# Performance work log

Hardware: AMD Instinct MI355X
Metric: run time of the kernel (lower is better)

Reference implementation:

```python
import jax, jax.numpy as jnp
import numpy as np
from jax import lax

EPOCHS = 3
KS = [2, 3, 4, 5]
GRID_D = 5           # sqrt(25): covariance viewed as 5x5 grid of flat indices
M_OUT = 18           # AttentionManifold output SPD size

def _sub_idx(d, k):
    # flat indices of k*k x k*k principal submatrices (stride-1 windows), per SubManifold
    starts = np.arange(0, d - k + 1)
    ir, ic = np.meshgrid(starts, starts, indexing='ij')
    base = (ir * d + ic).reshape(-1)                       # [num_windows]
    a, b = np.meshgrid(np.arange(k), np.arange(k), indexing='ij')
    rel = (a * d + b).reshape(-1)                          # [k*k]
    return base[:, None] + rel[None, :]                    # [num_windows, k*k]

SUB_IDX = [_sub_idx(GRID_D, k) for k in KS]
IN_DIMS = [k * k for k in KS]                              # [4, 9, 16, 25]
IU = np.triu_indices(M_OUT)                                # 171 tangent features
TRI_COEF = np.where(IU[0] == IU[1], 1.0, np.sqrt(2.0)).astype(np.float32)

def _sym_fn(x, fn):
    w, u = jnp.linalg.eigh(x)
    return jnp.einsum('...ik,...k,...jk->...ij', u, fn(w), u)

def spd_log(x, floor=1e-9):
    # matrix log of SPD matrix (== torch.svd-based log for PD input)
    return _sym_fn(x, lambda w: jnp.log(jnp.clip(w, floor)))

def spd_exp(x):
    return _sym_fn(x, jnp.exp)

def spd_rect(x, eps=1e-4):
    # SPDRectified (ReEig): clamp eigenvalues from below
    return _sym_fn(x, lambda w: jnp.clip(w, eps))

def bimap(X, W):
    # SPDTransform: W^T X W, W: [d_in, d_out]
    return jnp.einsum('ia,...ij,jb->...ab', W, X, W)

def diag_jitter(x):
    # deterministic analogue of the random diagonal jitter in SubmanifoldAttention.tensor_log
    n = x.shape[-1]
    return x + jnp.diag((1e-4 / n) * (1.0 + jnp.arange(n, dtype=x.dtype)))

def signal2spd(x):
    # x: [B, C, T] -> trace-normalized covariance [B, C, C]
    x = x - x.mean(-1, keepdims=True)
    cov = jnp.einsum('bct,bdt->bcd', x, x) / (x.shape[-1] - 1)
    tra = jnp.trace(cov, axis1=-2, axis2=-1)[:, None, None]
    cov = cov / tra
    return cov + 1e-5 * jnp.eye(cov.shape[-1], dtype=cov.dtype)

def spd_attention(Q, K, V, jitter):
    # log-maps computed once per element; pairwise log-Euclidean distance via Frobenius identity
    if jitter:
        Q, K, V = diag_jitter(Q), diag_jitter(K), diag_jitter(V)
    logQ, logK = spd_log(Q), spd_log(K)
    qn = jnp.sum(logQ * logQ, (-2, -1))                    # [B, m]
    kn = jnp.sum(logK * logK, (-2, -1))
    cross = jnp.einsum('bixy,bjxy->bij', logK, logQ)
    # E[b,i,j] = ||logQ_j - logK_i||_F^2  (sum of singular values of D D^T)
    E = jnp.maximum(kn[:, :, None] + qn[:, None, :] - 2.0 * cross, 0.0)
    score = 1.0 / (1.0 + jnp.log1p(E))
    P = jnp.swapaxes(jax.nn.softmax(score, axis=-2), -1, -2)  # softmax over i, then permute
    B, m, sz, _ = V.shape
    logV = spd_log(V).reshape(B, m, sz * sz)
    out_log = (P @ logV).reshape(B, m, sz, sz)             # log-Euclidean weighted mean
    out_log = 0.5 * (out_log + jnp.swapaxes(out_log, -1, -2))
    return spd_exp(out_log)

def _bn(y, g, b, m, v):
    inv = g / jnp.sqrt(v + 1e-5)
    return (y - m[None, :, None, None]) * inv[None, :, None, None] + b[None, :, None, None]

def _forward(x, c1w, c1b, bn1g, bn1b, bn1m, bn1v, c2w, c2b, bn2g, bn2b, bn2m, bn2v,
             sq0, sq1, sq2, sq3, sk0, sk1, sk2, sk3, sv0, sv1, sv2, sv3,
             mq, mk, mv, lw, lb):
    dn = ('NCHW', 'OIHW', 'NCHW')
    y = lax.conv_general_dilated(x, c1w, (1, 1), 'VALID', dimension_numbers=dn) + c1b[None, :, None, None]
    y = _bn(y, bn1g, bn1b, bn1m, bn1v)
    y = lax.conv_general_dilated(y, c2w, (1, 1), [(0, 0), (6, 6)], dimension_numbers=dn) + c2b[None, :, None, None]
    y = _bn(y, bn2g, bn2b, bn2m, bn2v)
    sig = y[:, :, 0, :]                                    # squeeze -> [B, 25, T+1]
    T = sig.shape[-1]
    base = T // EPOCHS
    lens = [base + (1 if i < T - base * EPOCHS else 0) for i in range(EPOCHS)]
    covs, off = [], 0
    for Lp in lens:
        covs.append(signal2spd(sig[..., off:off + Lp])); off += Lp
    covs = jnp.stack(covs, axis=1)                         # [B, 3, 25, 25]
    sqs = [sq0, sq1, sq2, sq3]; sks = [sk0, sk1, sk2, sk3]; svs = [sv0, sv1, sv2, sv3]
    branch = []
    for t in range(EPOCHS):
        xb = covs[:, t]                                    # [B, 25, 25]
        Qs, Ks, Vs = [], [], []
        for gi, idx in enumerate(SUB_IDX):
            sub = xb[:, idx[:, :, None], idx[:, None, :]]  # [B, nw, k*k, k*k]
            Qs.append(bimap(sub, sqs[gi]))
            Ks.append(bimap(sub, sks[gi]))
            Vs.append(bimap(sub, svs[gi]))
        att = spd_attention(jnp.concatenate(Qs, 1), jnp.concatenate(Ks, 1),
                            jnp.concatenate(Vs, 1), jitter=True)   # [B, 30, 25, 25]
        branch.append(spd_rect(att[:, -1]))                # keep_only_last
    xm = jnp.stack(branch, axis=1)                         # [B, 3, 25, 25]
    att2 = spd_attention(bimap(xm, mq), bimap(xm, mk), bimap(xm, mv), jitter=False)
    Lg = spd_log(spd_rect(att2))                           # [B, 3, 18, 18]
    feat = (Lg[..., IU[0], IU[1]] * jnp.asarray(TRI_COEF)).reshape(xm.shape[0], -1)
    return feat @ lw.T + lb                                # [B, 4]

def setup_inputs():
    B, T = 256, 1000
    key = jax.random.key(0)
    ks = jax.random.split(key, 40)
    def ortho(k, din, dout):
        a = jax.random.normal(k, (max(din, dout), min(din, dout)), dtype=jnp.float32)
        q, _ = jnp.linalg.qr(a)
        return q if din >= dout else q.T
    inp = {
        'x': jax.random.normal(ks[0], (B, 1, 22, T), dtype=jnp.float32),
        'c1w': 0.1 * jax.random.normal(ks[1], (22, 1, 22, 1), dtype=jnp.float32),
        'c1b': 0.01 * jax.random.normal(ks[2], (22,), dtype=jnp.float32),
        'bn1g': 1.0 + 0.1 * jax.random.normal(ks[3], (22,), dtype=jnp.float32),
        'bn1b': 0.01 * jax.random.normal(ks[4], (22,), dtype=jnp.float32),
        'bn1m': 0.1 * jax.random.normal(ks[5], (22,), dtype=jnp.float32),
        'bn1v': 0.5 + jax.random.uniform(ks[6], (22,), dtype=jnp.float32),
        'c2w': 0.05 * jax.random.normal(ks[7], (25, 22, 1, 12), dtype=jnp.float32),
        'c2b': 0.01 * jax.random.normal(ks[8], (25,), dtype=jnp.float32),
        'bn2g': 1.0 + 0.1 * jax.random.normal(ks[9], (25,), dtype=jnp.float32),
        'bn2b': 0.01 * jax.random.normal(ks[10], (25,), dtype=jnp.float32),
        'bn2m': 0.1 * jax.random.normal(ks[11], (25,), dtype=jnp.float32),
        'bn2v': 0.5 + jax.random.uniform(ks[12], (25,), dtype=jnp.float32),
    }
    for i, din in enumerate(IN_DIMS):
        inp[f'sq{i}'] = ortho(ks[13 + i], din, 4)
        inp[f'sk{i}'] = ortho(ks[17 + i], din, 4)
        inp[f'sv{i}'] = ortho(ks[21 + i], din, 25)
    inp['mq'] = ortho(ks[25], 25, 18)
    inp['mk'] = ortho(ks[26], 25, 18)
    inp['mv'] = ortho(ks[27], 25, 18)
    inp['lw'] = 0.05 * jax.random.normal(ks[28], (4, EPOCHS * len(IU[0])), dtype=jnp.float32)
    inp['lb'] = 0.01 * jax.random.normal(ks[29], (4,), dtype=jnp.float32)
    return inp

def reference(x, c1w, c1b, bn1g, bn1b, bn1m, bn1v, c2w, c2b, bn2g, bn2b, bn2m, bn2v,
              sq0, sq1, sq2, sq3, sk0, sk1, sk2, sk3, sv0, sv1, sv2, sv3,
              mq, mk, mv, lw, lb):
    return _forward(x, c1w, c1b, bn1g, bn1b, bn1m, bn1v, c2w, c2b, bn2g, bn2b, bn2m, bn2v,
                    sq0, sq1, sq2, sq3, sk0, sk1, sk2, sk3, sv0, sv1, sv2, sv3,
                    mq, mk, mv, lw, lb)
```

## Files before the change

kernel.cpp:

```cpp
#include <hip/hip_runtime.h>
#include <hip/hip_bf16.h>
#include <math.h>


__global__ __launch_bounds__(256) void conv1_kernel(
    const float* __restrict__ x, const float* __restrict__ c1w, const float* __restrict__ c1b,
    const float* __restrict__ g, const float* __restrict__ be, const float* __restrict__ mu,
    const float* __restrict__ va, float* __restrict__ ybn1)
{
  __shared__ float w[484];
  __shared__ float scl[22], sft[22];
  int t = threadIdx.x;
  for (int e = t; e < 484; e += 256) w[e] = c1w[e];
  if (t < 22) { float inv = g[t] / sqrtf(va[t] + 1e-5f); scl[t] = inv; sft[t] = be[t] - mu[t]*inv; }
  __syncthreads();
  int gid = blockIdx.x*256 + t;
  int b = gid / 1000, wp = gid % 1000;
  const float* xb = x + (size_t)b*22000 + wp;
  float acc[22];
  #pragma unroll
  for (int o = 0; o < 22; ++o) acc[o] = c1b[o];
  for (int h = 0; h < 22; ++h) {
    float xv = xb[h*1000];
    #pragma unroll
    for (int o = 0; o < 22; ++o) acc[o] += xv * w[o*22 + h];
  }
  float* yb = ybn1 + (size_t)b*22000 + wp;
  #pragma unroll
  for (int o = 0; o < 22; ++o) yb[o*1000] = acc[o]*scl[o] + sft[o];
}

__global__ __launch_bounds__(256) void conv2_kernel(
    const float* __restrict__ ybn1, const float* __restrict__ c2w, const float* __restrict__ c2b,
    const float* __restrict__ g, const float* __restrict__ be, const float* __restrict__ mu,
    const float* __restrict__ va, float* __restrict__ sig)
{
  __shared__ float w[6600];
  __shared__ float scl[25], sft[25];
  int t = threadIdx.x;
  for (int e = t; e < 6600; e += 256) w[e] = c2w[e];
  if (t < 25) { float inv = g[t] / sqrtf(va[t] + 1e-5f); scl[t] = inv; sft[t] = be[t] - mu[t]*inv; }
  __syncthreads();
  int gid = blockIdx.x*256 + t;
  if (gid >= 256*1001) return;
  int b = gid / 1001, wp = gid % 1001;
  const float* yb = ybn1 + (size_t)b*22000;
  float acc[25];
  #pragma unroll
  for (int p = 0; p < 25; ++p) acc[p] = c2b[p];
  for (int c = 0; c < 22; ++c) {
    for (int kw = 0; kw < 12; ++kw) {
      int wi = wp - 6 + kw;
      if (wi < 0 || wi >= 1000) continue;
      float v = yb[c*1000 + wi];
      #pragma unroll
      for (int p = 0; p < 25; ++p) acc[p] += v * w[p*264 + c*12 + kw];
    }
  }
  float* sb = sig + (size_t)b*25025 + wp;
  #pragma unroll
  for (int p = 0; p < 25; ++p) sb[p*1001] = acc[p]*scl[p] + sft[p];
}

__global__ __launch_bounds__(256) void spd_kernel(const float* __restrict__ sig, float* __restrict__ covs)
{
  __shared__ float s[25*334];
  __shared__ float mean[25];
  __shared__ float cv[625];
  __shared__ float tra;
  int bt = blockIdx.x; int b = bt/3, ep = bt%3;
  int off = ep*334;
  int Lp = (ep < 2) ? 334 : 333;
  int t = threadIdx.x;
  const float* sb = sig + (size_t)b*25025;
  for (int e = t; e < 25*Lp; e += 256) { int c = e / Lp, tt = e % Lp; s[c*334 + tt] = sb[c*1001 + off + tt]; }
  __syncthreads();
  if (t < 25) { float m = 0.f; for (int i = 0; i < Lp; ++i) m += s[t*334 + i]; mean[t] = m / (float)Lp; }
  __syncthreads();
  for (int pi = t; pi < 325; pi += 256) {
    int i = 0, rem = pi;
    while (rem >= 25 - i) { rem -= 25 - i; ++i; }
    int j = i + rem;
    float mi = mean[i], mj = mean[j], acc = 0.f;
    for (int k = 0; k < Lp; ++k) acc += (s[i*334 + k] - mi) * (s[j*334 + k] - mj);
    float v = acc / (float)(Lp - 1);
    cv[i*25 + j] = v; cv[j*25 + i] = v;
  }
  __syncthreads();
  if (t == 0) { float tr = 0.f; for (int i = 0; i < 25; ++i) tr += cv[i*26]; tra = tr; }
  __syncthreads();
  float inv = 1.f / tra;
  for (int e = t; e < 625; e += 256) {
    int i = e / 25, j = e % 25;
    covs[(size_t)bt*625 + e] = cv[e]*inv + ((i == j) ? 1e-5f : 0.f);
  }
}

__global__ __launch_bounds__(64) void build_windows_kernel(
    const float* __restrict__ covs,
    const float* __restrict__ sk0, const float* __restrict__ sk1, const float* __restrict__ sk2, const float* __restrict__ sk3,
    const float* __restrict__ sv0, const float* __restrict__ sv1, const float* __restrict__ sv2, const float* __restrict__ sv3,
    const float* __restrict__ sq3,
    float* __restrict__ Vbuf, float* __restrict__ Kbuf, float* __restrict__ Qbuf)
{
  __shared__ float sSub[625], sSv[625], sTmp[625], sSk[100], sTk[100];
  int bw = blockIdx.x;
  int bt = bw / 30, win = bw % 30;
  int t = threadIdx.x;
  int k, r0, c0;
  const float* sv; const float* sk;
  if (win < 16)      { k = 2; r0 = win/4;        c0 = win%4;        sv = sv0; sk = sk0; }
  else if (win < 25) { k = 3; int u = win-16; r0 = u/3; c0 = u%3;   sv = sv1; sk = sk1; }
  else if (win < 29) { k = 4; int u = win-25; r0 = u/2; c0 = u%2;   sv = sv2; sk = sk2; }
  else               { k = 5; r0 = 0;            c0 = 0;            sv = sv3; sk = sk3; }
  int kk = k*k;
  const float* cov = covs + (size_t)bt*625;
  for (int e = t; e < kk*kk; e += 64) {
    int p = e / kk, q = e % kk;
    int ip = (r0 + p/k)*5 + (c0 + p%k);
    int iq = (r0 + q/k)*5 + (c0 + q%k);
    sSub[p*kk + q] = cov[ip*25 + iq];
  }
  for (int e = t; e < kk*25; e += 64) sSv[e] = sv[e];
  for (int e = t; e < kk*4; e += 64)  sSk[e] = sk[e];
  __syncthreads();
  for (int e = t; e < kk*25; e += 64) {
    int i = e / 25, b = e % 25;
    float acc = 0.f;
    for (int j = 0; j < kk; ++j) acc += sSub[i*kk + j] * sSv[j*25 + b];
    sTmp[e] = acc;
  }
  for (int e = t; e < kk*4; e += 64) {
    int i = e / 4, b = e % 4;
    float acc = 0.f;
    for (int j = 0; j < kk; ++j) acc += sSub[i*kk + j] * sSk[j*4 + b];
    sTk[e] = acc;
  }
  __syncthreads();
  float* Vout = Vbuf + (size_t)bw*625;
  for (int e = t; e < 625; e += 64) {
    int a = e / 25, b = e % 25;
    float acc = 0.f;
    for (int i = 0; i < kk; ++i) acc += sSv[i*25 + a] * sTmp[i*25 + b];
    if (a == b) acc += 4e-6f * (float)(1 + a);
    Vout[e] = acc;
  }
  float* Kout = Kbuf + (size_t)bw*16;
  for (int e = t; e < 16; e += 64) {
    int a = e / 4, b = e % 4;
    float acc = 0.f;
    for (int i = 0; i < kk; ++i) acc += sSk[i*4 + a] * sTk[i*4 + b];
    if (a == b) acc += 2.5e-5f * (float)(1 + a);
    Kout[e] = acc;
  }
  if (win == 29) {
    __syncthreads();
    for (int e = t; e < 100; e += 64) {
      int i = e / 4, b = e % 4;
      float acc = 0.f;
      for (int j = 0; j < 25; ++j) acc += sSub[i*25 + j] * sq3[j*4 + b];
      sTk[e] = acc;
    }
    __syncthreads();
    float* Qout = Qbuf + (size_t)bt*16;
    for (int e = t; e < 16; e += 64) {
      int a = e / 4, b = e % 4;
      float acc = 0.f;
      for (int i = 0; i < 25; ++i) acc += sq3[i*4 + a] * sTk[i*4 + b];
      if (a == b) acc += 2.5e-5f * (float)(1 + a);
      Qout[e] = acc;
    }
  }
}

template<int NDATA, int MODE, int SHIFT>
__global__ __launch_bounds__(64) void eighreg_kernel(float* __restrict__ mats, float* __restrict__ norms_out)
{
  constexpr int NPAD = (NDATA + 1) & ~1;
  constexpr int NR   = NPAD - 1;
  constexpr int LDW  = NPAD + 1;
  constexpr int NT   = NDATA*(NDATA+1)/2;

  __shared__ float lds[2*NDATA*LDW];
  __shared__ float wvs[64];

  int t = threadIdx.x;
  int half = t >> 5;
  int col  = t & 31;
  int base32 = t & 32;
  float* M = mats + (size_t)blockIdx.x*2*NDATA*NDATA;

  for (int e = t; e < 2*NDATA*NDATA; e += 64) lds[e] = M[e];
  __syncthreads();

  const float* st = lds + half*NDATA*NDATA;
  float own[NDATA];
  float n_own = 0.f;
  #pragma unroll
  for (int r = 0; r < NDATA; ++r) {
    float v = 0.f;
    if (col < NDATA) {
      v = 0.5f*(st[r*NDATA + col] + st[col*NDATA + r]);
      if (r == col) v += (float)SHIFT;
    }
    own[r] = v;
    n_own += v*v;
  }
  __syncthreads();

  for (int sw = 0; sw < 12; ++sw) {
    float relacc = 0.f;
    #pragma unroll 1
    for (int r = 0; r < NR; ++r) {
      int p2 = 2*r - col;
      p2 += (p2 < 0) ? NR : 0;
      p2 -= (p2 >= NR) ? NR : 0;
      p2 = (col == r) ? (NPAD-1) : p2;
      p2 = (col == NPAD-1) ? r : p2;
      int idx = (base32 + p2) * 4;
      float y[NDATA];
      float d = 0.f;
      #pragma unroll
      for (int r2 = 0; r2 < NDATA; ++r2) {
        float yv = __int_as_float(__builtin_amdgcn_ds_bpermute(idx, __float_as_int(own[r2])));
        y[r2] = yv;
        d = fmaf(own[r2], yv, d);
      }
      float n_other = __int_as_float(__builtin_amdgcn_ds_bpermute(idx, __float_as_int(n_own)));
      float ad = fabsf(d);
      float dd = (ad > 1e-36f) ? d : 1e-36f;
      float tau = (n_other - n_own) * 0.5f * __builtin_amdgcn_rcpf(dd);
      float mag = __builtin_amdgcn_rcpf(fabsf(tau) + sqrtf(tau*tau + 1.f));
      float tt = copysignf(mag, tau);
      float c = __builtin_amdgcn_rsqf(tt*tt + 1.f);
      float s = tt * c;
      #pragma unroll
      for (int r2 = 0; r2 < NDATA; ++r2) own[r2] = c*own[r2] - s*y[r2];
      relacc = fmaxf(relacc, d*d * __builtin_amdgcn_rcpf(fmaxf(n_own*n_other, 1e-30f)));
      n_own = c*c*n_own + s*s*n_other - 2.f*c*s*d;
    }
    float nn = 0.f;
    #pragma unroll
    for (int r2 = 0; r2 < NDATA; ++r2) nn = fmaf(own[r2], own[r2], nn);
    n_own = nn;
    if (sw >= 1 && !__any(relacc >= 9e-10f)) break;
  }

  float lam = sqrtf(n_own) - (float)SHIFT;
  float f;
  if (MODE == 0)      f = logf(fmaxf(lam, 1e-9f));
  else if (MODE == 1) f = fmaxf(expf(lam), 1e-4f);
  else                f = fmaxf(lam, -9.210340371976182f);
  wvs[t] = (n_own < 1e-30f) ? 0.f : f * __builtin_amdgcn_rcpf(n_own);

  float* gn = lds + half*NDATA*LDW;
  if (col < NPAD) {
    #pragma unroll
    for (int r2 = 0; r2 < NDATA; ++r2) gn[r2*LDW + col] = own[r2];
  }
  __syncthreads();

  const float* wm = wvs + base32;
  float* Mo = M + half*NDATA*NDATA;
  float nacc = 0.f;
  for (int e = col; e < NT; e += 32) {
    int i = 0, rem = e;
    while (rem >= NDATA - i) { rem -= NDATA - i; ++i; }
    int j = i + rem;
    float acc = 0.f;
    #pragma unroll
    for (int k = 0; k < NDATA; ++k) acc += wm[k]*gn[i*LDW + k]*gn[j*LDW + k];
    Mo[i*NDATA + j] = acc;
    Mo[j*NDATA + i] = acc;
    nacc += (i == j) ? acc*acc : 2.f*acc*acc;
  }
  if (norms_out != nullptr) {
    #pragma unroll
    for (int o = 16; o > 0; o >>= 1) nacc += __shfl_xor(nacc, o);
    if (col == 0) norms_out[blockIdx.x*2 + half] = nacc;
  }
}

template<int P, int Q>
__device__ __forceinline__ void rot4(float a[4][4], float u[4][4])
{
  float apq = a[P][Q];
  if (fabsf(apq) < 1e-36f) return;
  float app = a[P][P], aqq = a[Q][Q];
  float tau = (aqq - app) / (2.f*apq);
  float tt = 1.f / (fabsf(tau) + sqrtf(tau*tau + 1.f));
  if (tau < 0.f) tt = -tt;
  float c = 1.f / sqrtf(tt*tt + 1.f), s = tt*c;
  #pragma unroll
  for (int k = 0; k < 4; ++k) { float akp = a[k][P], akq = a[k][Q]; a[k][P] = c*akp - s*akq; a[k][Q] = s*akp + c*akq; }
  #pragma unroll
  for (int k = 0; k < 4; ++k) { float apk = a[P][k], aqk = a[Q][k]; a[P][k] = c*apk - s*aqk; a[Q][k] = s*apk + c*aqk; }
  #pragma unroll
  for (int k = 0; k < 4; ++k) { float ukp = u[k][P], ukq = u[k][Q]; u[k][P] = c*ukp - s*ukq; u[k][Q] = s*ukp + c*ukq; }
}

__global__ __launch_bounds__(256) void eigh4_kernel(float* __restrict__ kmats, float* __restrict__ qmats,
                                                    float* __restrict__ norms)
{
  int idx = blockIdx.x*256 + threadIdx.x;
  if (idx >= 23808) return;
  float* M = (idx < 23040) ? (kmats + (size_t)idx*16) : (qmats + (size_t)(idx - 23040)*16);
  float a[4][4], u[4][4];
  #pragma unroll
  for (int i = 0; i < 4; ++i)
    #pragma unroll
    for (int j = 0; j < 4; ++j) { a[i][j] = 0.5f*(M[i*4+j] + M[j*4+i]); u[i][j] = (i == j) ? 1.f : 0.f; }
  #pragma unroll 1
  for (int sw = 0; sw < 8; ++sw) {
    rot4<0,1>(a,u); rot4<0,2>(a,u); rot4<0,3>(a,u);
    rot4<1,2>(a,u); rot4<1,3>(a,u); rot4<2,3>(a,u);
  }
  float f[4];
  #pragma unroll
  for (int i = 0; i < 4; ++i) f[i] = logf(fmaxf(a[i][i], 1e-9f));
  float nrm = 0.f;
  #pragma unroll
  for (int i = 0; i < 4; ++i)
    #pragma unroll
    for (int j = 0; j < 4; ++j) {
      float acc = 0.f;
      #pragma unroll
      for (int k = 0; k < 4; ++k) acc += u[i][k]*f[k]*u[j][k];
      M[i*4+j] = acc; nrm += acc*acc;
    }
  norms[idx] = nrm;
}

__global__ __launch_bounds__(64) void att1_kernel(
    const float* __restrict__ logK, const float* __restrict__ logQ,
    const float* __restrict__ kn, const float* __restrict__ qn,
    const float* __restrict__ logV, float* __restrict__ outlog1)
{
  __shared__ float lq[16];
  __shared__ float sscore[30];
  __shared__ float sp[30];
  int bt = blockIdx.x, t = threadIdx.x;
  if (t < 16) lq[t] = logQ[(size_t)bt*16 + t];
  __syncthreads();
  if (t < 30) {
    const float* lk = logK + ((size_t)bt*30 + t)*16;
    float cr = 0.f;
    #pragma unroll
    for (int e = 0; e < 16; ++e) cr += lk[e]*lq[e];
    float E = fmaxf(kn[bt*30 + t] + qn[bt] - 2.f*cr, 0.f);
    sscore[t] = 1.f/(1.f + log1pf(E));
  }
  __syncthreads();
  float mx = -1e30f;
  for (int i = 0; i < 30; ++i) mx = fmaxf(mx, sscore[i]);
  float sm = 0.f;
  for (int i = 0; i < 30; ++i) sm += expf(sscore[i] - mx);
  if (t < 30) sp[t] = expf(sscore[t] - mx)/sm;
  __syncthreads();
  const float* lv = logV + (size_t)bt*30*625;
  float* outp = outlog1 + (size_t)bt*625;
  for (int e = t; e < 625; e += 64) {
    float acc = 0.f;
    for (int i = 0; i < 30; ++i) acc += sp[i]*lv[(size_t)i*625 + e];
    outp[e] = acc;
  }
}

__global__ __launch_bounds__(64) void qkv2_kernel(
    const float* __restrict__ xm, const float* __restrict__ mq, const float* __restrict__ mk,
    const float* __restrict__ mv, float* __restrict__ q2, float* __restrict__ k2, float* __restrict__ v2)
{
  __shared__ float sx[625], sw[450], stmp[450];
  int bt = blockIdx.x, t = threadIdx.x;
  for (int e = t; e < 625; e += 64) sx[e] = xm[(size_t)bt*625 + e];
  for (int wi = 0; wi < 3; ++wi) {
    const float* W = (wi == 0) ? mq : (wi == 1) ? mk : mv;
    float* O = ((wi == 0) ? q2 : (wi == 1) ? k2 : v2) + (size_t)bt*324;
    for (int e = t; e < 450; e += 64) sw[e] = W[e];
    __syncthreads();
    for (int e = t; e < 450; e += 64) {
      int i = e / 18, b = e % 18;
      float acc = 0.f;
      for (int j = 0; j < 25; ++j) acc += sx[i*25 + j]*sw[j*18 + b];
      stmp[e] = acc;
    }
    __syncthreads();
    for (int e = t; e < 324; e += 64) {
      int a = e / 18, b = e % 18;
      float acc = 0.f;
      for (int i = 0; i < 25; ++i) acc += sw[i*18 + a]*stmp[i*18 + b];
      O[e] = acc;
    }
    __syncthreads();
  }
}

__global__ __launch_bounds__(64) void att2_kernel(
    const float* __restrict__ logQ2, const float* __restrict__ logK2, const float* __restrict__ logV2,
    const float* __restrict__ norms, float* __restrict__ outlog2)
{
  __shared__ float S[3][3];
  __shared__ float PT[3][3];
  int b = blockIdx.x, t = threadIdx.x;
  if (t < 9) {
    int i = t / 3, j = t % 3;
    const float* lk = logK2 + ((size_t)b*3 + i)*324;
    const float* lq = logQ2 + ((size_t)b*3 + j)*324;
    float cr = 0.f;
    for (int e = 0; e < 324; ++e) cr += lk[e]*lq[e];
    float E = fmaxf(norms[768 + b*3 + i] + norms[b*3 + j] - 2.f*cr, 0.f);
    S[i][j] = 1.f/(1.f + log1pf(E));
  }
  __syncthreads();
  if (t < 3) {
    float m = fmaxf(S[0][t], fmaxf(S[1][t], S[2][t]));
    float e0 = expf(S[0][t]-m), e1 = expf(S[1][t]-m), e2 = expf(S[2][t]-m);
    float ssum = e0 + e1 + e2;
    PT[t][0] = e0/ssum; PT[t][1] = e1/ssum; PT[t][2] = e2/ssum;
  }
  __syncthreads();
  for (int e = t; e < 324; e += 64) {
    float l0 = logV2[((size_t)b*3 + 0)*324 + e];
    float l1 = logV2[((size_t)b*3 + 1)*324 + e];
    float l2 = logV2[((size_t)b*3 + 2)*324 + e];
    #pragma unroll
    for (int j = 0; j < 3; ++j)
      outlog2[((size_t)b*3 + j)*324 + e] = PT[j][0]*l0 + PT[j][1]*l1 + PT[j][2]*l2;
  }
}

__global__ __launch_bounds__(64) void feat_kernel(
    const float* __restrict__ Lg, const float* __restrict__ lw, const float* __restrict__ lb,
    float* __restrict__ outp)
{
  __shared__ int tri_i[171], tri_j[171];
  int b = blockIdx.x, t = threadIdx.x;
  if (t == 0) { int f = 0; for (int i = 0; i < 18; ++i) for (int j = i; j < 18; ++j) { tri_i[f] = i; tri_j[f] = j; ++f; } }
  __syncthreads();
  float a0 = 0.f, a1 = 0.f, a2 = 0.f, a3 = 0.f;
  const float SQ2 = 1.41421356237309515f;
  for (int f = t; f < 513; f += 64) {
    int tt = f / 171, r = f % 171;
    int i = tri_i[r], j = tri_j[r];
    float coef = (i == j) ? 1.f : SQ2;
    float v = Lg[((size_t)b*3 + tt)*324 + i*18 + j] * coef;
    a0 += v*lw[0*513 + f]; a1 += v*lw[1*513 + f]; a2 += v*lw[2*513 + f]; a3 += v*lw[3*513 + f];
  }
  #pragma unroll
  for (int off = 32; off > 0; off >>= 1) {
    a0 += __shfl_down(a0, off); a1 += __shfl_down(a1, off);
    a2 += __shfl_down(a2, off); a3 += __shfl_down(a3, off);
  }
  if (t == 0) {
    outp[b*4 + 0] = a0 + lb[0]; outp[b*4 + 1] = a1 + lb[1];
    outp[b*4 + 2] = a2 + lb[2]; outp[b*4 + 3] = a3 + lb[3];
  }
}

extern "C" void kernel_launch(void* const* d_in, const int* in_sizes, int n_in,
                              void* d_out, int out_size, void* d_ws, size_t ws_size,
                              hipStream_t stream)
{
  const float* x    = (const float*)d_in[0];
  const float* c1w  = (const float*)d_in[1];
  const float* c1b  = (const float*)d_in[2];
  const float* bn1g = (const float*)d_in[3];
  const float* bn1b = (const float*)d_in[4];
  const float* bn1m = (const float*)d_in[5];
  const float* bn1v = (const float*)d_in[6];
  const float* c2w  = (const float*)d_in[7];
  const float* c2b  = (const float*)d_in[8];
  const float* bn2g = (const float*)d_in[9];
  const float* bn2b = (const float*)d_in[10];
  const float* bn2m = (const float*)d_in[11];
  const float* bn2v = (const float*)d_in[12];
  const float* sk0  = (const float*)d_in[14];
  const float* sv0  = (const float*)d_in[15];
  const float* sk1  = (const float*)d_in[17];
  const float* sv1  = (const float*)d_in[18];
  const float* sk2  = (const float*)d_in[20];
  const float* sv2  = (const float*)d_in[21];
  const float* sq3  = (const float*)d_in[22];
  const float* sk3  = (const float*)d_in[23];
  const float* sv3  = (const float*)d_in[24];
  const float* mq   = (const float*)d_in[25];
  const float* mk   = (const float*)d_in[26];
  const float* mv   = (const float*)d_in[27];
  const float* lw   = (const float*)d_in[28];
  const float* lb   = (const float*)d_in[29];
  float* outp = (float*)d_out;

  float* ws = (float*)d_ws;
  float* covs = ws;
  float* ybn1 = ws + 480000;
  float* sig  = ws + 6112000;
  float* Vbuf = ws + 480000;
  float* Kbuf = ws + 14880000;
  float* Qbuf = ws + 15248640;
  float* knb  = ws + 15260928;
  float* ol1  = ws + 15284736;
  float* qkv2 = ws + 15764736;
  float* nrm2 = ws + 16511232;
  float* ol2  = ws + 16513536;

  conv1_kernel<<<1000, 256, 0, stream>>>(x, c1w, c1b, bn1g, bn1b, bn1m, bn1v, ybn1);
  conv2_kernel<<<1001, 256, 0, stream>>>(ybn1, c2w, c2b, bn2g, bn2b, bn2m, bn2v, sig);
  spd_kernel<<<768, 256, 0, stream>>>(sig, covs);
  build_windows_kernel<<<23040, 64, 0, stream>>>(covs, sk0, sk1, sk2, sk3, sv0, sv1, sv2, sv3, sq3,
                                                 Vbuf, Kbuf, Qbuf);
  eighreg_kernel<25,0,0><<<11520, 64, 0, stream>>>(Vbuf, nullptr);
  eigh4_kernel<<<93, 256, 0, stream>>>(Kbuf, Qbuf, knb);
  att1_kernel<<<768, 64, 0, stream>>>(Kbuf, Qbuf, knb, knb + 23040, Vbuf, ol1);
  eighreg_kernel<25,1,16><<<384, 64, 0, stream>>>(ol1, nullptr);
  qkv2_kernel<<<768, 64, 0, stream>>>(ol1, mq, mk, mv, qkv2, qkv2 + 248832, qkv2 + 497664);
  eighreg_kernel<18,0,0><<<1152, 64, 0, stream>>>(qkv2, nrm2);
  att2_kernel<<<256, 64, 0, stream>>>(qkv2, qkv2 + 248832, qkv2 + 497664, nrm2, ol2);
  eighreg_kernel<18,2,16><<<384, 64, 0, stream>>>(ol2, nullptr);
  feat_kernel<<<256, 64, 0, stream>>>(ol2, lw, lb, outp);
}
```

Before: 1.430 ms.

## Rewrite one-sided Jacobi eigensolver to hold two columns per lane with DPP rotation

The eigensolver now packs four matrices per 64-lane block, with each lane holding a pair of columns in registers. Instead of a bpermute exchange of a whole column every round, it rotates the pair in place and uses a DPP row shift to pass columns around a round-robin ring. This removes most LDS permute traffic and halves the number of blocks. In exchange it raises register pressure, since two 25-element columns are kept per lane, and it changes the convergence test and tolerance.

```diff
diff --git a/kernel.cpp b/kernel.cpp
--- a/kernel.cpp
+++ b/kernel.cpp
@@ -173,111 +173,171 @@
   }
 }
 
+__device__ __forceinline__ float dpp_prev(float v) {
+  return __int_as_float(__builtin_amdgcn_update_dpp(0, __float_as_int(v), 0x111, 0xF, 0xF, true));
+}
+__device__ __forceinline__ float dpp_next(float v) {
+  return __int_as_float(__builtin_amdgcn_update_dpp(0, __float_as_int(v), 0x101, 0xF, 0xF, true));
+}
+
 template<int NDATA, int MODE, int SHIFT>
-__global__ __launch_bounds__(64) void eighreg_kernel(float* __restrict__ mats, float* __restrict__ norms_out)
-{
-  constexpr int NPAD = (NDATA + 1) & ~1;
-  constexpr int NR   = NPAD - 1;
-  constexpr int LDW  = NPAD + 1;
-  constexpr int NT   = NDATA*(NDATA+1)/2;
-
-  __shared__ float lds[2*NDATA*LDW];
-  __shared__ float wvs[64];
+__global__ __launch_bounds__(64) void eighbl_kernel(float* __restrict__ mats, float* __restrict__ norms_out)
+{
+  constexpr int ND    = NDATA;
+  constexpr int NPAIR = (NDATA+1)/2;
+  constexpr int NPAD  = 2*NPAIR;
+  constexpr int NRND  = NPAD-1;
+  constexpr int NT    = ND*(ND+1)/2;
+  constexpr int STG   = 4*ND*ND;
+  constexpr int GNS   = 4*NPAD*ND;
+  constexpr int LSZ   = (STG > GNS ? STG : GNS);
+
+  __shared__ float lds[LSZ];
+  __shared__ float wv[4*NPAD];
 
   int t = threadIdx.x;
-  int half = t >> 5;
-  int col  = t & 31;
-  int base32 = t & 32;
-  float* M = mats + (size_t)blockIdx.x*2*NDATA*NDATA;
-
-  for (int e = t; e < 2*NDATA*NDATA; e += 64) lds[e] = M[e];
-  __syncthreads();
-
-  const float* st = lds + half*NDATA*NDATA;
-  float own[NDATA];
-  float n_own = 0.f;
-  #pragma unroll
-  for (int r = 0; r < NDATA; ++r) {
-    float v = 0.f;
-    if (col < NDATA) {
-      v = 0.5f*(st[r*NDATA + col] + st[col*NDATA + r]);
-      if (r == col) v += (float)SHIFT;
-    }
-    own[r] = v;
-    n_own += v*v;
-  }
-  __syncthreads();
-
+  int rl = t & 15, mat = t >> 4;
+  bool act = rl < NPAIR;
+  bool is0 = rl == 0;
+  bool isL = rl == NPAIR-1;
+  float* M = mats + (size_t)blockIdx.x*4*ND*ND;
+
+  for (int e = t; e < STG; e += 64) lds[e] = M[e];
+  __syncthreads();
+
+  const float* st = lds + mat*ND*ND;
+  int cA = rl, cB = rl + NPAIR;
+  float a[ND], b[ND];
+  float na = 0.f, nb = 0.f;
+  #pragma unroll
+  for (int i = 0; i < ND; ++i) {
+    float va = 0.f, vb = 0.f;
+    if (act) {
+      va = 0.5f*(st[i*ND + cA] + st[cA*ND + i]);
+      if (i == cA) va += (float)SHIFT;
+      if (cB < ND) {
+        vb = 0.5f*(st[i*ND + cB] + st[cB*ND + i]);
+        if (i == cB) vb += (float)SHIFT;
+      }
+    }
+    a[i] = va; b[i] = vb;
+    na += va*va; nb += vb*vb;
+  }
+
+  const float TOL2 = 4e-8f;
   for (int sw = 0; sw < 12; ++sw) {
-    float relacc = 0.f;
+    int bad = 0;
     #pragma unroll 1
-    for (int r = 0; r < NR; ++r) {
-      int p2 = 2*r - col;
-      p2 += (p2 < 0) ? NR : 0;
-      p2 -= (p2 >= NR) ? NR : 0;
-      p2 = (col == r) ? (NPAD-1) : p2;
-      p2 = (col == NPAD-1) ? r : p2;
-      int idx = (base32 + p2) * 4;
-      float y[NDATA];
-      float d = 0.f;
+    for (int r = 0; r < NRND; ++r) {
+      float d0=0.f,d1=0.f,d2=0.f,d3=0.f,d4=0.f;
       #pragma unroll
-      for (int r2 = 0; r2 < NDATA; ++r2) {
-        float yv = __int_as_float(__builtin_amdgcn_ds_bpermute(idx, __float_as_int(own[r2])));
-        y[r2] = yv;
-        d = fmaf(own[r2], yv, d);
+      for (int i = 0; i < ND; ++i) {
+        float pr = a[i]*b[i];
+        if      (i % 5 == 0) d0 += pr;
+        else if (i % 5 == 1) d1 += pr;
+        else if (i % 5 == 2) d2 += pr;
+        else if (i % 5 == 3) d3 += pr;
+        else                 d4 += pr;
       }
-      float n_other = __int_as_float(__builtin_amdgcn_ds_bpermute(idx, __float_as_int(n_own)));
+      float d = ((d0 + d1) + (d2 + d3)) + d4;
       float ad = fabsf(d);
       float dd = (ad > 1e-36f) ? d : 1e-36f;
-      float tau = (n_other - n_own) * 0.5f * __builtin_amdgcn_rcpf(dd);
+      float tau = (nb - na) * 0.5f * __builtin_amdgcn_rcpf(dd);
       float mag = __builtin_amdgcn_rcpf(fabsf(tau) + sqrtf(tau*tau + 1.f));
       float tt = copysignf(mag, tau);
       float c = __builtin_amdgcn_rsqf(tt*tt + 1.f);
       float s = tt * c;
       #pragma unroll
-      for (int r2 = 0; r2 < NDATA; ++r2) own[r2] = c*own[r2] - s*y[r2];
-      relacc = fmaxf(relacc, d*d * __builtin_amdgcn_rcpf(fmaxf(n_own*n_other, 1e-30f)));
-      n_own = c*c*n_own + s*s*n_other - 2.f*c*s*d;
-    }
-    float nn = 0.f;
-    #pragma unroll
-    for (int r2 = 0; r2 < NDATA; ++r2) nn = fmaf(own[r2], own[r2], nn);
-    n_own = nn;
-    if (sw >= 1 && !__any(relacc >= 9e-10f)) break;
-  }
-
-  float lam = sqrtf(n_own) - (float)SHIFT;
-  float f;
-  if (MODE == 0)      f = logf(fmaxf(lam, 1e-9f));
-  else if (MODE == 1) f = fmaxf(expf(lam), 1e-4f);
-  else                f = fmaxf(lam, -9.210340371976182f);
-  wvs[t] = (n_own < 1e-30f) ? 0.f : f * __builtin_amdgcn_rcpf(n_own);
-
-  float* gn = lds + half*NDATA*LDW;
-  if (col < NPAD) {
-    #pragma unroll
-    for (int r2 = 0; r2 < NDATA; ++r2) gn[r2*LDW + col] = own[r2];
-  }
-  __syncthreads();
-
-  const float* wm = wvs + base32;
-  float* Mo = M + half*NDATA*NDATA;
+      for (int i = 0; i < ND; ++i) {
+        float ta = a[i];
+        a[i] = c*ta - s*b[i];
+        b[i] = s*ta + c*b[i];
+      }
+      float csd = 2.f*c*s*d;
+      float nan_ = c*c*na + s*s*nb - csd;
+      float nbn_ = s*s*na + c*c*nb + csd;
+      bad |= (act && (d*d > TOL2*na*nb)) ? 1 : 0;
+      na = nan_; nb = nbn_;
+      #pragma unroll
+      for (int i = 0; i < ND; ++i) {
+        float tA = dpp_prev(a[i]);
+        float tB = dpp_next(b[i]);
+        float ao = a[i];
+        a[i] = is0 ? tB : tA;
+        b[i] = isL ? ao : (is0 ? b[i] : tB);
+      }
+      {
+        float tA = dpp_prev(na);
+        float tB = dpp_next(nb);
+        float ao = na;
+        na = is0 ? tB : tA;
+        nb = isL ? ao : (is0 ? nb : tB);
+      }
+    }
+    {
+      float n0=0.f,n1=0.f,n2=0.f,n3=0.f,n4=0.f;
+      float m0=0.f,m1=0.f,m2=0.f,m3=0.f,m4=0.f;
+      #pragma unroll
+      for (int i = 0; i < ND; ++i) {
+        float pa = a[i]*a[i], pb = b[i]*b[i];
+        if      (i % 5 == 0) { n0 += pa; m0 += pb; }
+        else if (i % 5 == 1) { n1 += pa; m1 += pb; }
+        else if (i % 5 == 2) { n2 += pa; m2 += pb; }
+        else if (i % 5 == 3) { n3 += pa; m3 += pb; }
+        else                 { n4 += pa; m4 += pb; }
+      }
+      na = ((n0 + n1) + (n2 + n3)) + n4;
+      nb = ((m0 + m1) + (m2 + m3)) + m4;
+    }
+    if (sw >= 1 && !__any(bad)) break;
+  }
+
+  float lamA = sqrtf(na) - (float)SHIFT;
+  float lamB = sqrtf(nb) - (float)SHIFT;
+  float fA, fB;
+  if (MODE == 0)      { fA = logf(fmaxf(lamA, 1e-9f));  fB = logf(fmaxf(lamB, 1e-9f)); }
+  else if (MODE == 1) { fA = fmaxf(expf(lamA), 1e-4f);  fB = fmaxf(expf(lamB), 1e-4f); }
+  else                { fA = fmaxf(lamA, -9.210340371976182f); fB = fmaxf(lamB, -9.210340371976182f); }
+  float wA = (na < 1e-30f) ? 0.f : fA * __builtin_amdgcn_rcpf(na);
+  float wB = (nb < 1e-30f) ? 0.f : fB * __builtin_amdgcn_rcpf(nb);
+
+  __syncthreads();
+  float* gn = lds + mat*NPAD*ND;
+  if (act) {
+    #pragma unroll
+    for (int i = 0; i < ND; ++i) {
+      gn[rl*ND + i] = a[i];
+      gn[(rl + NPAIR)*ND + i] = b[i];
+    }
+    wv[mat*NPAD + rl] = wA;
+    wv[mat*NPAD + rl + NPAIR] = wB;
+  }
+  __syncthreads();
+
+  float wreg[NPAD];
+  #pragma unroll
+  for (int k = 0; k < NPAD; ++k) wreg[k] = wv[mat*NPAD + k];
+
+  float* Mo = M + mat*ND*ND;
+  const float* g = lds + mat*NPAD*ND;
   float nacc = 0.f;
-  for (int e = col; e < NT; e += 32) {
+  for (int e = rl; e < NT; e += 16) {
     int i = 0, rem = e;
-    while (rem >= NDATA - i) { rem -= NDATA - i; ++i; }
+    while (rem >= ND - i) { rem -= ND - i; ++i; }
     int j = i + rem;
     float acc = 0.f;
     #pragma unroll
-    for (int k = 0; k < NDATA; ++k) acc += wm[k]*gn[i*LDW + k]*gn[j*LDW + k];
-    Mo[i*NDATA + j] = acc;
-    Mo[j*NDATA + i] = acc;
+    for (int k = 0; k < NPAD; ++k) acc += wreg[k] * g[k*ND + i] * g[k*ND + j];
+    Mo[i*ND + j] = acc;
+    Mo[j*ND + i] = acc;
     nacc += (i == j) ? acc*acc : 2.f*acc*acc;
   }
   if (norms_out != nullptr) {
-    #pragma unroll
-    for (int o = 16; o > 0; o >>= 1) nacc += __shfl_xor(nacc, o);
-    if (col == 0) norms_out[blockIdx.x*2 + half] = nacc;
+    nacc += __shfl_xor(nacc, 8);
+    nacc += __shfl_xor(nacc, 4);
+    nacc += __shfl_xor(nacc, 2);
+    nacc += __shfl_xor(nacc, 1);
+    if (rl == 0) norms_out[blockIdx.x*4 + mat] = nacc;
   }
 }
 
@@ -508,13 +568,13 @@
   spd_kernel<<<768, 256, 0, stream>>>(sig, covs);
   build_windows_kernel<<<23040, 64, 0, stream>>>(covs, sk0, sk1, sk2, sk3, sv0, sv1, sv2, sv3, sq3,
                                                  Vbuf, Kbuf, Qbuf);
-  eighreg_kernel<25,0,0><<<11520, 64, 0, stream>>>(Vbuf, nullptr);
+  eighbl_kernel<25,0,0><<<5760, 64, 0, stream>>>(Vbuf, nullptr);
   eigh4_kernel<<<93, 256, 0, stream>>>(Kbuf, Qbuf, knb);
   att1_kernel<<<768, 64, 0, stream>>>(Kbuf, Qbuf, knb, knb + 23040, Vbuf, ol1);
-  eighreg_kernel<25,1,16><<<384, 64, 0, stream>>>(ol1, nullptr);
+  eighbl_kernel<25,1,16><<<192, 64, 0, stream>>>(ol1, nullptr);
   qkv2_kernel<<<768, 64, 0, stream>>>(ol1, mq, mk, mv, qkv2, qkv2 + 248832, qkv2 + 497664);
-  eighreg_kernel<18,0,0><<<1152, 64, 0, stream>>>(qkv2, nrm2);
+  eighbl_kernel<18,0,0><<<576, 64, 0, stream>>>(qkv2, nrm2);
   att2_kernel<<<256, 64, 0, stream>>>(qkv2, qkv2 + 248832, qkv2 + 497664, nrm2, ol2);
-  eighreg_kernel<18,2,16><<<384, 64, 0, stream>>>(ol2, nullptr);
+  eighbl_kernel<18,2,16><<<192, 64, 0, stream>>>(ol2, nullptr);
   feat_kernel<<<256, 64, 0, stream>>>(ol2, lw, lb, outp);
 }
```

New measurement: 1.372 ms. 4.1% less time.
